# Optimization experiments

Measured on AMD Instinct MI355X. Metric: run time of the kernel, lower is better.

## Reference

```python
import jax, jax.numpy as jnp
import numpy as np

N_HEADS = 16
POOL_WIDTH = 3


def setup_inputs() -> dict:
    key = jax.random.key(0)
    ks = jax.random.split(key, 6)
    B, S, D = 4, 1024, 1024
    x = jax.random.normal(ks[0], (B, S, D), dtype=jnp.float32)
    W_q = jax.random.normal(ks[1], (D, D), dtype=jnp.float32) * 0.02
    W_k = jax.random.normal(ks[2], (D, D), dtype=jnp.float32) * 0.02
    W_v = jax.random.normal(ks[3], (D, D), dtype=jnp.float32) * 0.02
    W_o = jax.random.normal(ks[4], (D, D), dtype=jnp.float32) * 0.02
    freq_raw = jnp.zeros((D,), dtype=jnp.float32)
    pool_raw = jnp.array([0.25, 1.0, 0.25], dtype=jnp.float32)
    return {"x": x, "W_q": W_q, "W_k": W_k, "W_v": W_v, "W_o": W_o,
            "freq_raw": freq_raw, "pool_raw": pool_raw}


def _spectral_attention(x, W_q, W_k, W_v, W_o, freq_raw, pool_raw):
    B, S, D = x.shape
    H = N_HEADS
    hd = D // H
    pw = POOL_WIDTH
    pad = pw // 2

    # projections (torch Linear: y = x @ W.T)
    Q = x @ W_q.T
    K = x @ W_k.T
    V = x @ W_v.T

    # monotone non-increasing freq weights: reverse cumsum of softplus
    fw = jnp.flip(jnp.cumsum(jnp.flip(jax.nn.softplus(freq_raw))))
    # symmetric, positive pool weights
    pwts = jax.nn.softplus((pool_raw + jnp.flip(pool_raw)) * 0.5)

    Qh = (Q * fw).reshape(B, S, H, hd).transpose(0, 2, 1, 3)  # [B,H,S,hd]
    K_pad = jnp.pad(K, ((0, 0), (0, 0), (pad, pad)))          # [B,S,D+2*pad]

    scores = jnp.zeros((B, H, S, S), dtype=x.dtype)
    for i in range(pw):  # small fixed loop over pool offsets
        K_shift = jax.lax.dynamic_slice_in_dim(K_pad, i, D, axis=2)
        Kh = K_shift.reshape(B, S, H, hd).transpose(0, 2, 1, 3)
        scores = scores + pwts[i] * jnp.einsum('bhqd,bhkd->bhqk', Qh, Kh)
    scores = scores / np.sqrt(hd).astype(x.dtype)

    causal = jnp.tril(jnp.ones((S, S), dtype=bool))
    scores = jnp.where(causal, scores, jnp.finfo(scores.dtype).min)
    attn = jax.nn.softmax(scores, axis=-1)

    Vh = V.reshape(B, S, H, hd).transpose(0, 2, 1, 3)
    out = jnp.einsum('bhqk,bhkd->bhqd', attn, Vh)
    out = out.transpose(0, 2, 1, 3).reshape(B, S, D)
    return out @ W_o.T


def reference(x, W_q, W_k, W_v, W_o, freq_raw, pool_raw):
    return _spectral_attention(x, W_q, W_k, W_v, W_o, freq_raw, pool_raw)
```

## Files before the change

### kernel.cpp

```cpp
#include <hip/hip_runtime.h>

typedef __attribute__((ext_vector_type(8))) short short8;
typedef __attribute__((ext_vector_type(4))) float float4v;
typedef __attribute__((ext_vector_type(4))) float floatx4;
typedef __attribute__((ext_vector_type(4))) unsigned short ushort4v;

#define DEV static __device__ __forceinline__
#define MFMA __builtin_amdgcn_mfma_f32_16x16x32_bf16

DEV unsigned short f2bf(float f){
  unsigned u = __builtin_bit_cast(unsigned, f);
  unsigned r = u + 0x7FFFu + ((u >> 16) & 1u);
  return (unsigned short)(r >> 16);
}
DEV float bf2f(unsigned short h){
  unsigned u = ((unsigned)h) << 16;
  return __builtin_bit_cast(float, u);
}
DEV float softplus_f(float x){
  if (x > 20.f) return x;
  return log1pf(expf(x));
}

DEV void gload16(const void* g, void* l){
  __builtin_amdgcn_global_load_lds(
      (const __attribute__((address_space(1))) unsigned int*)g,
      (__attribute__((address_space(3))) unsigned int*)l, 16, 0, 0);
}

__global__ void k_prep_fw(const float* __restrict__ freq_raw,
                          const float* __restrict__ pool_raw,
                          float* __restrict__ fw, float* __restrict__ pw){
  __shared__ float s[1024];
  int d = threadIdx.x;
  s[d] = softplus_f(freq_raw[d]);
  __syncthreads();
  for (int off = 1; off < 1024; off <<= 1){
    float t = (d + off < 1024) ? s[d + off] : 0.f;
    __syncthreads();
    s[d] += t;
    __syncthreads();
  }
  fw[d] = s[d];
  if (d < 3) pw[d] = softplus_f((pool_raw[d] + pool_raw[2 - d]) * 0.5f);
}

__global__ __launch_bounds__(256) void k_prep_w(
    const float* __restrict__ Wq, const float* __restrict__ Wk,
    const float* __restrict__ Wv, const float* __restrict__ Wo,
    const float* __restrict__ fw, const float* __restrict__ pw,
    unsigned short* __restrict__ wq_h, unsigned short* __restrict__ wq_l,
    unsigned short* __restrict__ wk_h, unsigned short* __restrict__ wk_l,
    unsigned short* __restrict__ wv_b, unsigned short* __restrict__ wo_b){
  int idx = blockIdx.x * 256 + threadIdx.x;
  int n  = idx >> 8;
  int k4 = (idx & 255) << 2;
  float p0 = pw[0], p1 = pw[1], p2 = pw[2];
  float f = fw[n] * 0.125f;
  int o = n * 1024 + k4;
  float4v q4 = *(const float4v*)(Wq + o);
  float4v k0v = *(const float4v*)(Wk + o);
  float4v km = {0.f,0.f,0.f,0.f}, kp = {0.f,0.f,0.f,0.f};
  if (n > 0)    km = *(const float4v*)(Wk + o - 1024);
  if (n < 1023) kp = *(const float4v*)(Wk + o + 1024);
  float4v v4 = *(const float4v*)(Wv + o);
  float4v o4 = *(const float4v*)(Wo + o);
  ushort4v qh, ql, kh, kl, vb, ob;
  for (int j = 0; j < 4; j++){
    float wq_ = f * q4[j];
    unsigned short h = f2bf(wq_);
    qh[j] = h; ql[j] = f2bf(wq_ - bf2f(h));
    float wk_ = p0 * km[j] + p1 * k0v[j] + p2 * kp[j];
    h = f2bf(wk_);
    kh[j] = h; kl[j] = f2bf(wk_ - bf2f(h));
    vb[j] = f2bf(v4[j]);
    ob[j] = f2bf(o4[j]);
  }
  *(ushort4v*)(wq_h + o) = qh; *(ushort4v*)(wq_l + o) = ql;
  *(ushort4v*)(wk_h + o) = kh; *(ushort4v*)(wk_l + o) = kl;
  *(ushort4v*)(wv_b + o) = vb; *(ushort4v*)(wo_b + o) = ob;
}

__global__ __launch_bounds__(256) void k_split_x(const float* __restrict__ x,
                                                 unsigned short* __restrict__ xh,
                                                 unsigned short* __restrict__ xl){
  int idx = blockIdx.x * 256 + threadIdx.x;
  int o = idx * 4;
  float4v v = *(const float4v*)(x + o);
  ushort4v h4, l4;
  for (int j = 0; j < 4; j++){
    unsigned short h = f2bf(v[j]);
    h4[j] = h; l4[j] = f2bf(v[j] - bf2f(h));
  }
  *(ushort4v*)(xh + o) = h4;
  *(ushort4v*)(xl + o) = l4;
}

__global__ __launch_bounds__(256) void k_qkv(
    const unsigned short* __restrict__ Ah, const unsigned short* __restrict__ Al,
    const unsigned short* __restrict__ Bqh, const unsigned short* __restrict__ Bql,
    const unsigned short* __restrict__ Bkh, const unsigned short* __restrict__ Bkl,
    const unsigned short* __restrict__ Bvh,
    unsigned short* __restrict__ qh_o, unsigned short* __restrict__ ql_o,
    unsigned short* __restrict__ kh_o, unsigned short* __restrict__ kl_o,
    unsigned short* __restrict__ vt_o){
  __shared__ unsigned short lds[2][18432];
  int tid = threadIdx.x;
  int w = tid >> 6, l = tid & 63, lg = l >> 4, lr = l & 15;
  int wr = w >> 1, wc = w & 1;
  int g = blockIdx.x;
  int mblk = (g & 7) * 4 + ((g >> 3) & 3);
  int nblk = g >> 5;
  int m0 = mblk * 128, n0 = nblk * 64;

  auto stage = [&](int kt, int bufi){
    unsigned short* buf = lds[bufi];
    for (int rep = 0; rep < 2; rep++){
      int idx = rep * 256 + tid;
      int r = idx >> 2, c = idx & 3;
      int cs = (c ^ ((r >> 1) & 3)) * 8;
      int srcA = (m0 + r) * 1024 + kt + cs;
      unsigned short* dst = buf + rep * 2048 + w * 512;
      gload16(Ah + srcA, dst);
      gload16(Al + srcA, dst + 4096);
    }
    {
      int r = tid >> 2, c = tid & 3;
      int cs = (c ^ ((r >> 1) & 3)) * 8;
      int srcB = (n0 + r) * 1024 + kt + cs;
      unsigned short* dst = buf + 8192 + w * 512;
      gload16(Bqh + srcB, dst);
      gload16(Bql + srcB, dst + 2048);
      gload16(Bkh + srcB, dst + 4096);
      gload16(Bkl + srcB, dst + 6144);
      gload16(Bvh + srcB, dst + 8192);
    }
  };

  floatx4 aq[4][2] = {}, ak[4][2] = {}, av[4][2] = {};
  stage(0, 0);
  __syncthreads();
  int cur = 0;
  for (int kt = 0; kt < 1024; kt += 32){
    if (kt + 32 < 1024) stage(kt + 32, cur ^ 1);
    const unsigned short* buf = lds[cur];
    short8 a_h[4], a_l[4], bq_h[2], bq_l[2], bk_h[2], bk_l[2], bv_h[2];
    #pragma unroll
    for (int ms = 0; ms < 4; ms++){
      int r = wr * 64 + ms * 16 + lr;
      int off = r * 32 + ((lg ^ ((r >> 1) & 3)) * 8);
      a_h[ms] = *(const short8*)(buf + off);
      a_l[ms] = *(const short8*)(buf + 4096 + off);
    }
    #pragma unroll
    for (int ns = 0; ns < 2; ns++){
      int r = wc * 32 + ns * 16 + lr;
      int off = r * 32 + ((lg ^ ((r >> 1) & 3)) * 8);
      bq_h[ns] = *(const short8*)(buf + 8192 + off);
      bq_l[ns] = *(const short8*)(buf + 10240 + off);
      bk_h[ns] = *(const short8*)(buf + 12288 + off);
      bk_l[ns] = *(const short8*)(buf + 14336 + off);
      bv_h[ns] = *(const short8*)(buf + 16384 + off);
    }
    #pragma unroll
    for (int ms = 0; ms < 4; ms++)
      #pragma unroll
      for (int ns = 0; ns < 2; ns++){
        aq[ms][ns] = MFMA(a_h[ms], bq_h[ns], aq[ms][ns], 0, 0, 0);
        aq[ms][ns] = MFMA(a_h[ms], bq_l[ns], aq[ms][ns], 0, 0, 0);
        aq[ms][ns] = MFMA(a_l[ms], bq_h[ns], aq[ms][ns], 0, 0, 0);
        ak[ms][ns] = MFMA(a_h[ms], bk_h[ns], ak[ms][ns], 0, 0, 0);
        ak[ms][ns] = MFMA(a_h[ms], bk_l[ns], ak[ms][ns], 0, 0, 0);
        ak[ms][ns] = MFMA(a_l[ms], bk_h[ns], ak[ms][ns], 0, 0, 0);
        av[ms][ns] = MFMA(a_h[ms], bv_h[ns], av[ms][ns], 0, 0, 0);
      }
    __syncthreads();
    cur ^= 1;
  }
  for (int ms = 0; ms < 4; ms++)
    for (int ns = 0; ns < 2; ns++){
      int mrow = m0 + wr * 64 + ms * 16 + lg * 4;
      int ncol = n0 + wc * 32 + ns * 16 + lr;
      for (int rr = 0; rr < 4; rr++){
        int o = (mrow + rr) * 1024 + ncol;
        float v = aq[ms][ns][rr];
        unsigned short hh = f2bf(v);
        qh_o[o] = hh; ql_o[o] = f2bf(v - bf2f(hh));
        v = ak[ms][ns][rr];
        hh = f2bf(v);
        kh_o[o] = hh; kl_o[o] = f2bf(v - bf2f(hh));
      }
      int tb = m0 + wr * 64;
      int bq = tb >> 10, sg = (tb >> 6) & 15;
      int P0 = ((ms >> 1) << 5) | (lg << 3) | ((ms & 1) << 2);
      ushort4v v4;
      for (int rr = 0; rr < 4; rr++) v4[rr] = f2bf(av[ms][ns][rr]);
      *(ushort4v*)(vt_o + (ncol * 4 + bq) * 1024 + sg * 64 + P0) = v4;
    }
}

template<int OUT>
__global__ __launch_bounds__(256) void k_gemm(
    const unsigned short* __restrict__ Ah, const unsigned short* __restrict__ Bh,
    void* __restrict__ out0, int M, int N, int K){
  constexpr int BUFN = 6144;
  __shared__ unsigned short lds[3 * BUFN];
  int tid = threadIdx.x;
  int w = tid >> 6, l = tid & 63, lg = l >> 4, lr = l & 15;
  int wr = w >> 1, wc = w & 1;
  int n0 = blockIdx.x * 128, m0 = blockIdx.y * 64;

  auto stage = [&](int kt, int bufi){
    unsigned short* buf = lds + bufi * BUFN;
    { int r = tid >> 2, c = tid & 3;
      int src = (m0 + r) * K + kt + (c ^ ((r >> 1) & 3)) * 8;
      gload16(Ah + src, buf + w * 512); }
    for (int rep = 0; rep < 2; rep++){
      int idx = rep * 256 + tid;
      int r = idx >> 2, c = idx & 3;
      int src = (n0 + r) * K + kt + (c ^ ((r >> 1) & 3)) * 8;
      gload16(Bh + src, buf + 2048 + rep * 2048 + w * 512);
    }
  };

  floatx4 acc[2][4] = {};
  int nT = K >> 5;
  stage(0, 0);
  stage(32, 1);
  for (int t = 0; t < nT; ++t){
    if (t == nT - 1) asm volatile("s_waitcnt vmcnt(0)" ::: "memory");
    else             asm volatile("s_waitcnt vmcnt(3)" ::: "memory");
    __builtin_amdgcn_sched_barrier(0);
    __builtin_amdgcn_s_barrier();
    __builtin_amdgcn_sched_barrier(0);
    if (t + 2 < nT) stage((t + 2) * 32, (t + 2) % 3);

    const unsigned short* buf = lds + (t % 3) * BUFN;
    short8 a_h[2], b_h[4];
    #pragma unroll
    for (int ms = 0; ms < 2; ms++){
      int r = wr * 32 + ms * 16 + lr;
      int off = r * 32 + ((lg ^ ((r >> 1) & 3)) * 8);
      a_h[ms] = *(const short8*)(buf + off);
    }
    #pragma unroll
    for (int ns = 0; ns < 4; ns++){
      int r = wc * 64 + ns * 16 + lr;
      int off = r * 32 + ((lg ^ ((r >> 1) & 3)) * 8);
      b_h[ns] = *(const short8*)(buf + 2048 + off);
    }
    #pragma unroll
    for (int ms = 0; ms < 2; ms++)
      #pragma unroll
      for (int ns = 0; ns < 4; ns++)
        acc[ms][ns] = MFMA(a_h[ms], b_h[ns], acc[ms][ns], 0, 0, 0);
  }
  for (int ms = 0; ms < 2; ms++)
    for (int ns = 0; ns < 4; ns++){
      int mrow = m0 + wr * 32 + ms * 16 + lg * 4;
      int ncol = n0 + wc * 64 + ns * 16 + lr;
      for (int rr = 0; rr < 4; rr++){
        float v = acc[ms][ns][rr];
        int o = (mrow + rr) * N + ncol;
        if constexpr (OUT == 2) ((float*)out0)[o] = v;
        else                    ((unsigned short*)out0)[o] = f2bf(v);
      }
    }
}

__global__ __launch_bounds__(256) void k_attn(
    const unsigned short* __restrict__ Qh, const unsigned short* __restrict__ Ql,
    const unsigned short* __restrict__ Kh, const unsigned short* __restrict__ Kl,
    const unsigned short* __restrict__ Vt, unsigned short* __restrict__ Ob){
  __shared__ unsigned short s_k[2][12288];
  int tid = threadIdx.x;
  int w = tid >> 6, l = tid & 63, lg = l >> 4, lr = l & 15;
  int gx = blockIdx.x;
  int bh = gx & 63, qt = gx >> 6;
  int b = bh >> 4, h = bh & 15;
  int q0 = qt * 64;
  int qs = q0 + w * 16;
  int rowb = b * 1024;

  auto stage = [&](int kt, int bufi){
    int k0 = kt * 64;
    unsigned short* buf = s_k[bufi];
    for (int rep = 0; rep < 2; rep++){
      int idx = rep * 256 + tid;
      int r = idx >> 3, c = idx & 7;
      int cs = c ^ (r & 7);
      int srcK = (rowb + k0 + r) * 1024 + h * 64 + cs * 8;
      int srcV = ((h * 64 + r) * 4 + b) * 1024 + k0 + cs * 8;
      unsigned short* dst = buf + rep * 2048 + w * 512;
      gload16(Kh + srcK, dst);
      gload16(Kl + srcK, dst + 4096);
      gload16(Vt + srcV, dst + 8192);
    }
  };

  short8 fqh[2], fql[2];
  for (int ds = 0; ds < 2; ds++){
    int off = (rowb + qs + lr) * 1024 + h * 64 + ds * 32 + lg * 8;
    fqh[ds] = *(const short8*)(Qh + off);
    fql[ds] = *(const short8*)(Ql + off);
  }

  floatx4 oT[4] = {};
  float m_r = -__builtin_inff(), l_r = 0.f;

  int ntile = qt + 1;
  stage(0, 0);
  __syncthreads();
  int cur = 0;
  for (int kt = 0; kt < ntile; kt++){
    int k0 = kt * 64;
    if (kt + 1 < ntile) stage(kt + 1, cur ^ 1);
    const unsigned short* kb = s_k[cur];

    floatx4 sc[4] = {};
    __builtin_amdgcn_s_setprio(1);
    for (int ds = 0; ds < 2; ds++)
      for (int s = 0; s < 4; s++){
        int r = s * 16 + lr;
        int off = r * 64 + (((ds * 4 + lg) ^ (r & 7)) * 8);
        short8 kh_f = *(const short8*)(kb + off);
        short8 kl_f = *(const short8*)(kb + 4096 + off);
        sc[s] = MFMA(kh_f, fqh[ds], sc[s], 0, 0, 0);
        sc[s] = MFMA(kl_f, fqh[ds], sc[s], 0, 0, 0);
        sc[s] = MFMA(kh_f, fql[ds], sc[s], 0, 0, 0);
      }
    __builtin_amdgcn_s_setprio(0);

    if (kt == ntile - 1){
      #pragma unroll
      for (int s = 0; s < 4; s++)
        #pragma unroll
        for (int rr = 0; rr < 4; rr++)
          if (k0 + s * 16 + 4 * lg + rr > qs + lr) sc[s][rr] = -__builtin_inff();
    }

    float mx = sc[0][0];
    #pragma unroll
    for (int s = 0; s < 4; s++)
      #pragma unroll
      for (int rr = 0; rr < 4; rr++) mx = fmaxf(mx, sc[s][rr]);
    mx = fmaxf(mx, __shfl_xor(mx, 16));
    mx = fmaxf(mx, __shfl_xor(mx, 32));
    float mn = fmaxf(m_r, mx);
    float fac = __expf(m_r - mn);
    m_r = mn;
    float ps = 0.f;
    #pragma unroll
    for (int s = 0; s < 4; s++)
      #pragma unroll
      for (int rr = 0; rr < 4; rr++){
        float p = __expf(sc[s][rr] - mn);
        sc[s][rr] = p;
        ps += p;
      }
    ps += __shfl_xor(ps, 16);
    ps += __shfl_xor(ps, 32);
    l_r = l_r * fac + ps;
    #pragma unroll
    for (int dsb = 0; dsb < 4; dsb++) oT[dsb] *= fac;

    __builtin_amdgcn_s_setprio(1);
    #pragma unroll
    for (int kk = 0; kk < 2; kk++){
      short8 pb;
      #pragma unroll
      for (int j = 0; j < 8; j++)
        pb[j] = (short)f2bf(sc[2 * kk + (j >> 2)][j & 3]);
      #pragma unroll
      for (int dsb = 0; dsb < 4; dsb++){
        int rv = dsb * 16 + lr;
        int offv = rv * 64 + (((kk * 4 + lg) ^ (rv & 7)) * 8);
        short8 vb = *(const short8*)(kb + 8192 + offv);
        oT[dsb] = MFMA(vb, pb, oT[dsb], 0, 0, 0);
      }
    }
    __builtin_amdgcn_s_setprio(0);
    __syncthreads();
    cur ^= 1;
  }

  float inv = 1.f / l_r;
  int base = (rowb + qs + lr) * 1024 + h * 64;
  #pragma unroll
  for (int dsb = 0; dsb < 4; dsb++){
    ushort4v o4;
    #pragma unroll
    for (int rr = 0; rr < 4; rr++) o4[rr] = f2bf(oT[dsb][rr] * inv);
    *(ushort4v*)(Ob + base + dsb * 16 + 4 * lg) = o4;
  }
}

extern "C" void kernel_launch(void* const* d_in, const int* in_sizes, int n_in,
                              void* d_out, int out_size, void* d_ws, size_t ws_size,
                              hipStream_t stream){
  const float* x  = (const float*)d_in[0];
  const float* Wq = (const float*)d_in[1];
  const float* Wk = (const float*)d_in[2];
  const float* Wv = (const float*)d_in[3];
  const float* Wo = (const float*)d_in[4];
  const float* fr = (const float*)d_in[5];
  const float* pr = (const float*)d_in[6];

  char* ws = (char*)d_ws;
  size_t off = 0;
  auto alloc = [&](size_t bytes) -> char* {
    char* p = ws + off;
    off += (bytes + 255) & ~(size_t)255;
    return p;
  };
  float* fw = (float*)alloc(1024 * sizeof(float));
  float* pw = (float*)alloc(256);
  const size_t WB = (size_t)1024 * 1024 * 2;
  unsigned short* wq_h = (unsigned short*)alloc(WB);
  unsigned short* wq_l = (unsigned short*)alloc(WB);
  unsigned short* wk_h = (unsigned short*)alloc(WB);
  unsigned short* wk_l = (unsigned short*)alloc(WB);
  unsigned short* wv_b = (unsigned short*)alloc(WB);
  unsigned short* wo_b = (unsigned short*)alloc(WB);
  const size_t XB = (size_t)4096 * 1024 * 2;
  unsigned short* x_h = (unsigned short*)alloc(XB);
  unsigned short* x_l = (unsigned short*)alloc(XB);
  unsigned short* q_h = (unsigned short*)alloc(XB);
  unsigned short* q_l = (unsigned short*)alloc(XB);
  unsigned short* k_h = (unsigned short*)alloc(XB);
  unsigned short* k_l = (unsigned short*)alloc(XB);
  unsigned short* vt  = (unsigned short*)alloc(XB);
  unsigned short* o_b = x_l;

  k_prep_fw<<<1, 1024, 0, stream>>>(fr, pr, fw, pw);
  k_prep_w<<<1024, 256, 0, stream>>>(Wq, Wk, Wv, Wo, fw, pw,
                                     wq_h, wq_l, wk_h, wk_l, wv_b, wo_b);
  k_split_x<<<4096, 256, 0, stream>>>(x, x_h, x_l);

  k_qkv<<<512, 256, 0, stream>>>(x_h, x_l, wq_h, wq_l, wk_h, wk_l, wv_b,
                                 q_h, q_l, k_h, k_l, vt);
  k_attn<<<1024, 256, 0, stream>>>(q_h, q_l, k_h, k_l, vt, o_b);
  dim3 ggo(8, 64);
  k_gemm<2><<<ggo, 256, 0, stream>>>(o_b, wo_b, d_out, 4096, 1024, 1024);
}
```

Measured before the change: 132.4 us.

## Fuse prep kernels into one launch and schedule heavy causal tiles first

Merges the frequency-weight scan, weight conversion and x split into a single kernel. Each weight-row block now recomputes its own reverse-cumsum entry with a block reduction instead of reading a serially scanned buffer, which removes two launches and their dependency chain at the cost of redundant softplus work. The attention kernel also reverses the query-tile order so that the longest causal tiles are dispatched first, which should reduce tail imbalance at the end of the grid.

```diff
diff --git a/kernel.cpp b/kernel.cpp
--- a/kernel.cpp
+++ b/kernel.cpp
@@ -28,72 +28,69 @@
       (__attribute__((address_space(3))) unsigned int*)l, 16, 0, 0);
 }
 
-__global__ void k_prep_fw(const float* __restrict__ freq_raw,
-                          const float* __restrict__ pool_raw,
-                          float* __restrict__ fw, float* __restrict__ pw){
-  __shared__ float s[1024];
-  int d = threadIdx.x;
-  s[d] = softplus_f(freq_raw[d]);
-  __syncthreads();
-  for (int off = 1; off < 1024; off <<= 1){
-    float t = (d + off < 1024) ? s[d + off] : 0.f;
-    __syncthreads();
-    s[d] += t;
-    __syncthreads();
-  }
-  fw[d] = s[d];
-  if (d < 3) pw[d] = softplus_f((pool_raw[d] + pool_raw[2 - d]) * 0.5f);
-}
-
-__global__ __launch_bounds__(256) void k_prep_w(
+__global__ __launch_bounds__(256) void k_prep(
+    const float* __restrict__ freq_raw, const float* __restrict__ pool_raw,
+    const float* __restrict__ x,
     const float* __restrict__ Wq, const float* __restrict__ Wk,
     const float* __restrict__ Wv, const float* __restrict__ Wo,
-    const float* __restrict__ fw, const float* __restrict__ pw,
     unsigned short* __restrict__ wq_h, unsigned short* __restrict__ wq_l,
     unsigned short* __restrict__ wk_h, unsigned short* __restrict__ wk_l,
-    unsigned short* __restrict__ wv_b, unsigned short* __restrict__ wo_b){
-  int idx = blockIdx.x * 256 + threadIdx.x;
-  int n  = idx >> 8;
-  int k4 = (idx & 255) << 2;
-  float p0 = pw[0], p1 = pw[1], p2 = pw[2];
-  float f = fw[n] * 0.125f;
-  int o = n * 1024 + k4;
-  float4v q4 = *(const float4v*)(Wq + o);
-  float4v k0v = *(const float4v*)(Wk + o);
-  float4v km = {0.f,0.f,0.f,0.f}, kp = {0.f,0.f,0.f,0.f};
-  if (n > 0)    km = *(const float4v*)(Wk + o - 1024);
-  if (n < 1023) kp = *(const float4v*)(Wk + o + 1024);
-  float4v v4 = *(const float4v*)(Wv + o);
-  float4v o4 = *(const float4v*)(Wo + o);
-  ushort4v qh, ql, kh, kl, vb, ob;
-  for (int j = 0; j < 4; j++){
-    float wq_ = f * q4[j];
-    unsigned short h = f2bf(wq_);
-    qh[j] = h; ql[j] = f2bf(wq_ - bf2f(h));
-    float wk_ = p0 * km[j] + p1 * k0v[j] + p2 * kp[j];
-    h = f2bf(wk_);
-    kh[j] = h; kl[j] = f2bf(wk_ - bf2f(h));
-    vb[j] = f2bf(v4[j]);
-    ob[j] = f2bf(o4[j]);
-  }
-  *(ushort4v*)(wq_h + o) = qh; *(ushort4v*)(wq_l + o) = ql;
-  *(ushort4v*)(wk_h + o) = kh; *(ushort4v*)(wk_l + o) = kl;
-  *(ushort4v*)(wv_b + o) = vb; *(ushort4v*)(wo_b + o) = ob;
-}
-
-__global__ __launch_bounds__(256) void k_split_x(const float* __restrict__ x,
-                                                 unsigned short* __restrict__ xh,
-                                                 unsigned short* __restrict__ xl){
-  int idx = blockIdx.x * 256 + threadIdx.x;
-  int o = idx * 4;
-  float4v v = *(const float4v*)(x + o);
-  ushort4v h4, l4;
-  for (int j = 0; j < 4; j++){
-    unsigned short h = f2bf(v[j]);
-    h4[j] = h; l4[j] = f2bf(v[j] - bf2f(h));
-  }
-  *(ushort4v*)(xh + o) = h4;
-  *(ushort4v*)(xl + o) = l4;
+    unsigned short* __restrict__ wv_b, unsigned short* __restrict__ wo_b,
+    unsigned short* __restrict__ xh, unsigned short* __restrict__ xl){
+  int g = blockIdx.x;
+  int tid = threadIdx.x;
+  if (g < 1024){
+    __shared__ float red[256];
+    int n = g;
+    float s = 0.f;
+    for (int j = tid; j < 1024; j += 256)
+      if (j >= n) s += softplus_f(freq_raw[j]);
+    red[tid] = s;
+    __syncthreads();
+    for (int off = 128; off > 0; off >>= 1){
+      if (tid < off) red[tid] += red[tid + off];
+      __syncthreads();
+    }
+    float f = red[0] * 0.125f;
+    float p0 = softplus_f((pool_raw[0] + pool_raw[2]) * 0.5f);
+    float p1 = softplus_f(pool_raw[1]);
+    float p2 = p0;
+
+    int k4 = tid << 2;
+    int o = n * 1024 + k4;
+    float4v q4 = *(const float4v*)(Wq + o);
+    float4v k0v = *(const float4v*)(Wk + o);
+    float4v km = {0.f,0.f,0.f,0.f}, kp = {0.f,0.f,0.f,0.f};
+    if (n > 0)    km = *(const float4v*)(Wk + o - 1024);
+    if (n < 1023) kp = *(const float4v*)(Wk + o + 1024);
+    float4v v4 = *(const float4v*)(Wv + o);
+    float4v o4 = *(const float4v*)(Wo + o);
+    ushort4v qh, ql, kh, kl, vb, ob;
+    for (int j = 0; j < 4; j++){
+      float wq_ = f * q4[j];
+      unsigned short h = f2bf(wq_);
+      qh[j] = h; ql[j] = f2bf(wq_ - bf2f(h));
+      float wk_ = p0 * km[j] + p1 * k0v[j] + p2 * kp[j];
+      h = f2bf(wk_);
+      kh[j] = h; kl[j] = f2bf(wk_ - bf2f(h));
+      vb[j] = f2bf(v4[j]);
+      ob[j] = f2bf(o4[j]);
+    }
+    *(ushort4v*)(wq_h + o) = qh; *(ushort4v*)(wq_l + o) = ql;
+    *(ushort4v*)(wk_h + o) = kh; *(ushort4v*)(wk_l + o) = kl;
+    *(ushort4v*)(wv_b + o) = vb; *(ushort4v*)(wo_b + o) = ob;
+  } else {
+    int idx = (g - 1024) * 256 + tid;
+    int o = idx * 4;
+    float4v v = *(const float4v*)(x + o);
+    ushort4v h4, l4;
+    for (int j = 0; j < 4; j++){
+      unsigned short h = f2bf(v[j]);
+      h4[j] = h; l4[j] = f2bf(v[j] - bf2f(h));
+    }
+    *(ushort4v*)(xh + o) = h4;
+    *(ushort4v*)(xl + o) = l4;
+  }
 }
 
 __global__ __launch_bounds__(256) void k_qkv(
@@ -276,7 +273,7 @@
   int tid = threadIdx.x;
   int w = tid >> 6, l = tid & 63, lg = l >> 4, lr = l & 15;
   int gx = blockIdx.x;
-  int bh = gx & 63, qt = gx >> 6;
+  int bh = gx & 63, qt = 15 - (gx >> 6);
   int b = bh >> 4, h = bh & 15;
   int q0 = qt * 64;
   int qs = q0 + w * 16;
@@ -413,8 +410,6 @@
     off += (bytes + 255) & ~(size_t)255;
     return p;
   };
-  float* fw = (float*)alloc(1024 * sizeof(float));
-  float* pw = (float*)alloc(256);
   const size_t WB = (size_t)1024 * 1024 * 2;
   unsigned short* wq_h = (unsigned short*)alloc(WB);
   unsigned short* wq_l = (unsigned short*)alloc(WB);
@@ -432,11 +427,9 @@
   unsigned short* vt  = (unsigned short*)alloc(XB);
   unsigned short* o_b = x_l;
 
-  k_prep_fw<<<1, 1024, 0, stream>>>(fr, pr, fw, pw);
-  k_prep_w<<<1024, 256, 0, stream>>>(Wq, Wk, Wv, Wo, fw, pw,
-                                     wq_h, wq_l, wk_h, wk_l, wv_b, wo_b);
-  k_split_x<<<4096, 256, 0, stream>>>(x, x_h, x_l);
-
+  k_prep<<<5120, 256, 0, stream>>>(fr, pr, x, Wq, Wk, Wv, Wo,
+                                   wq_h, wq_l, wk_h, wk_l, wv_b, wo_b,
+                                   x_h, x_l);
   k_qkv<<<512, 256, 0, stream>>>(x_h, x_l, wq_h, wq_l, wk_h, wk_l, wv_b,
                                  q_h, q_l, k_h, k_l, vt);
   k_attn<<<1024, 256, 0, stream>>>(q_h, q_l, k_h, k_l, vt, o_b);
```

Result: faster. 118.7 us (median of 3 runs) (-10.3%).
